# Optimization experiments

Measured on AMD Instinct MI355X. Metric: run time of the kernel, lower is better.

## Reference

```python
import jax, jax.numpy as jnp
import numpy as np

H = 1024
F = 4096  # base_ffn_dim = hidden * 4
WIDTHS = [256, 512]  # adapters; idx 2 -> width==hidden -> identity
EPS = 1e-5


def _xavier(key, fan_in, fan_out, gain):
    a = gain * np.sqrt(6.0 / (fan_in + fan_out))
    return jax.random.uniform(key, (fan_in, fan_out), jnp.float32, -a, a)


def _layernorm(x, g, b):
    mu = jnp.mean(x, axis=-1, keepdims=True)
    var = jnp.var(x, axis=-1, keepdims=True)
    return (x - mu) * jax.lax.rsqrt(var + EPS) * g + b


def setup_inputs() -> dict:
    key = jax.random.key(0)
    ks = jax.random.split(key, 12)
    g = 1.0 / np.sqrt(2.0)
    B, S = 4, 2048
    return {
        "x": jax.random.normal(ks[0], (B, S, H), jnp.float32),
        "width_multiplier": jax.random.uniform(ks[1], (B, S, 1), jnp.float32),
        "width_idx": jax.random.randint(ks[2], (B, S), 0, 3, jnp.int32),
        "ln_in_g": jnp.ones((H,), jnp.float32),
        "ln_in_b": jnp.zeros((H,), jnp.float32),
        "W1": _xavier(ks[3], H, F, g),
        "b1": jnp.zeros((F,), jnp.float32),
        "ln_h_g": jnp.ones((F,), jnp.float32),
        "ln_h_b": jnp.zeros((F,), jnp.float32),
        "W2": _xavier(ks[4], F, H, g),
        "b2": jnp.zeros((H,), jnp.float32),
        "a256_w1": _xavier(ks[5], H, 256, g),
        "a256_b1": jnp.zeros((256,), jnp.float32),
        "a256_w2": _xavier(ks[6], 256, H, g),
        "a256_b2": jnp.zeros((H,), jnp.float32),
        "a512_w1": _xavier(ks[7], H, 512, g),
        "a512_b1": jnp.zeros((512,), jnp.float32),
        "a512_w2": _xavier(ks[8], 512, H, g),
        "a512_b2": jnp.zeros((H,), jnp.float32),
    }


def reference(x, width_multiplier, width_idx,
              ln_in_g, ln_in_b, W1, b1, ln_h_g, ln_h_b, W2, b2,
              a256_w1, a256_b1, a256_w2, a256_b2,
              a512_w1, a512_b1, a512_w2, a512_b2):
    gelu = lambda t: jax.nn.gelu(t, approximate=False)  # torch nn.GELU exact
    x_norm = _layernorm(x, ln_in_g, ln_in_b)
    # base FFN path
    h = gelu(jnp.einsum("bsh,hf->bsf", x_norm, W1) + b1)
    h = _layernorm(h, ln_h_g, ln_h_b)
    base = jnp.einsum("bsf,fh->bsh", h, W2) + b2
    # width adapters (routed per token by width_idx)
    ad0 = jnp.einsum("bsw,wh->bsh", gelu(jnp.einsum("bsh,hw->bsw", x_norm, a256_w1) + a256_b1), a256_w2) + a256_b2
    ad1 = jnp.einsum("bsw,wh->bsh", gelu(jnp.einsum("bsh,hw->bsw", x_norm, a512_w1) + a512_b1), a512_w2) + a512_b2
    idx = width_idx[..., None]
    adaptive = jnp.where(idx == 0, ad0, jnp.where(idx == 1, ad1, x_norm))
    return base * width_multiplier + adaptive * (1.0 - width_multiplier)
```

## Files before the change

### kernel.cpp

```cpp
#include <hip/hip_runtime.h>
#include <cstdint>
#include <cstddef>

typedef unsigned short u16x8 __attribute__((ext_vector_type(8)));
typedef unsigned short u16x4 __attribute__((ext_vector_type(4)));
typedef __bf16 bf16x8 __attribute__((ext_vector_type(8)));
typedef float f32x4 __attribute__((ext_vector_type(4)));

__device__ __forceinline__ float b2f(unsigned short u) {
    union { unsigned int i; float f; } v;
    v.i = ((unsigned int)u) << 16;
    return v.f;
}

__device__ __forceinline__ unsigned short f2b(float f) {
    union { float f; unsigned int i; } v;
    v.f = f;
    unsigned int x = v.i;
    unsigned int lsb = (x >> 16) & 1u;
    x += 0x7FFFu + lsb;
    return (unsigned short)(x >> 16);
}

__device__ __forceinline__ float gelu_exact(float x) {
    return 0.5f * x * (1.0f + erff(x * 0.70710678118654752f));
}

__device__ __forceinline__ void ld_lds16(const unsigned short* g, unsigned short* l) {
    __builtin_amdgcn_global_load_lds(
        (const __attribute__((address_space(1))) void*)g,
        (__attribute__((address_space(3))) void*)l, 16, 0, 0);
}


__device__ __forceinline__ void transp_body(const float* __restrict__ in,
                                            unsigned short* __restrict__ out,
                                            int R, int C,
                                            const float* __restrict__ scale,
                                            int bx, int by) {
    __shared__ float tile[32][33];
    const int tx = threadIdx.x & 31;
    const int ty = threadIdx.x >> 5;
    int x = bx * 32 + tx;
    int y0 = by * 32;
    for (int k = 0; k < 32; k += 8)
        tile[ty + k][tx] = in[(size_t)(y0 + ty + k) * C + x];
    __syncthreads();
    int ox = y0 + tx;
    int oy = bx * 32;
    float sc = scale ? scale[ox] : 1.0f;
    for (int k = 0; k < 32; k += 8)
        out[(size_t)(oy + ty + k) * R + ox] = f2b(tile[tx][ty + k] * sc);
}

__device__ __forceinline__ void c01_partial_body(const float* __restrict__ W2,
                                                 const float* __restrict__ g,
                                                 const float* __restrict__ b,
                                                 float* __restrict__ pc0,
                                                 float* __restrict__ pc1,
                                                 int N, int kc, int nb) {
    int n = (nb << 8) + threadIdx.x;
    int k0 = kc << 8;
    float p0 = 0.f, p1 = 0.f;
    for (int k = k0; k < k0 + 256; ++k) {
        float w = W2[(size_t)k * N + n];
        p0 += b[k] * w;
        p1 += g[k] * w;
    }
    pc0[kc * 1024 + n] = p0;
    pc1[kc * 1024 + n] = p1;
}

__device__ __forceinline__ void ln1024_body(const float* __restrict__ in,
                                            unsigned short* __restrict__ out,
                                            const float* __restrict__ g,
                                            const float* __restrict__ b,
                                            int row) {
    const int t = threadIdx.x;
    f32x4 v = ((const f32x4*)(in + (size_t)row * 1024))[t];
    float s = v[0] + v[1] + v[2] + v[3];
    float s2 = v[0] * v[0] + v[1] * v[1] + v[2] * v[2] + v[3] * v[3];
#pragma unroll
    for (int o = 32; o > 0; o >>= 1) {
        s  += __shfl_down(s, o, 64);
        s2 += __shfl_down(s2, o, 64);
    }
    __shared__ float red[8];
    int lane = t & 63, w = t >> 6;
    if (lane == 0) { red[w] = s; red[4 + w] = s2; }
    __syncthreads();
    if (t == 0) {
        red[0] = red[0] + red[1] + red[2] + red[3];
        red[4] = red[4] + red[5] + red[6] + red[7];
    }
    __syncthreads();
    const float inv_n = 1.0f / 1024.0f;
    float mu = red[0] * inv_n;
    float var = red[4] * inv_n - mu * mu;
    float rs = rsqrtf(var + 1e-5f);
    f32x4 gv = ((const f32x4*)g)[t];
    f32x4 bv = ((const f32x4*)b)[t];
    u16x4 ov;
#pragma unroll
    for (int r = 0; r < 4; ++r) ov[r] = f2b((v[r] - mu) * rs * gv[r] + bv[r]);
    ((u16x4*)(out + (size_t)row * 1024))[t] = ov;
}

__device__ __forceinline__ void rowstats_body(const unsigned short* __restrict__ h,
                                              float* __restrict__ st, int row) {
    const int t = threadIdx.x;
    const u16x8* p = (const u16x8*)(h + (size_t)row * 4096);
    float s = 0.f, s2 = 0.f;
#pragma unroll
    for (int i = 0; i < 2; ++i) {
        u16x8 v = p[t + (i << 8)];
#pragma unroll
        for (int r = 0; r < 8; ++r) { float f = b2f(v[r]); s += f; s2 += f * f; }
    }
#pragma unroll
    for (int o = 32; o > 0; o >>= 1) {
        s  += __shfl_down(s, o, 64);
        s2 += __shfl_down(s2, o, 64);
    }
    __shared__ float red2[8];
    int lane = t & 63, w = t >> 6;
    if (lane == 0) { red2[w] = s; red2[4 + w] = s2; }
    __syncthreads();
    if (t == 0) {
        float ss = red2[0] + red2[1] + red2[2] + red2[3];
        float qq = red2[4] + red2[5] + red2[6] + red2[7];
        const float inv = 1.0f / 4096.0f;
        float mu = ss * inv;
        float var = qq * inv - mu * mu;
        float rs = rsqrtf(var + 1e-5f);
        st[2 * (size_t)row]     = rs;
        st[2 * (size_t)row + 1] = rs * mu;
    }
}

template <int EPI>
__device__ __forceinline__ void gemm_body(
    unsigned short (*As)[128 * 32], unsigned short (*Bs)[128 * 32],
    int fid, int nbx, int nby,
    const unsigned short* __restrict__ A, int lda,
    const unsigned short* __restrict__ BT, int ldb,
    const float* __restrict__ bias, unsigned short* __restrict__ Cb,
    float* __restrict__ Cf, int N, int K,
    const int* __restrict__ idx, int match,
    const float* __restrict__ wm,
    const unsigned short* __restrict__ adaptive,
    const unsigned short* __restrict__ xn,
    const float* __restrict__ c1v,
    const float* __restrict__ rstat) {
    const int t = threadIdx.x;

    int id = fid;
    const int nwg = nbx * nby;
    if ((nwg & 7) == 0) {
        const int cpx = nwg >> 3;
        id = (id & 7) * cpx + (id >> 3);
    }
    const int bx = id % nbx;
    const int by = id / nbx;
    const int m0 = by * 128;
    const int n0 = bx * 128;

    const int lane = t & 63;
    const int wid = t >> 6;

    const int srow = lane >> 2;
    const int sch  = (lane & 3) ^ (srow & 3);
    const int scol = sch << 3;

    const int wr = (wid >> 1) << 6;
    const int wc = (wid & 1) << 6;
    const int ml = lane & 15;
    const int q = lane >> 4;
    const int qsw = ((q ^ (ml & 3)) << 3);

    f32x4 acc[4][4];
#pragma unroll
    for (int i = 0; i < 4; ++i)
#pragma unroll
        for (int j = 0; j < 4; ++j)
#pragma unroll
            for (int r = 0; r < 4; ++r) acc[i][j][r] = 0.0f;

    const int nk = K >> 5;

#define STAGE(KT, BUF)                                                          \
    {                                                                           \
        _Pragma("unroll")                                                       \
        for (int hh = 0; hh < 2; ++hh) {                                        \
            int rbase = wid * 32 + hh * 16;                                     \
            int row = rbase + srow;                                             \
            ld_lds16(A  + (size_t)(m0 + row) * lda + (KT) * 32 + scol,          \
                     &As[BUF][rbase * 32]);                                     \
            ld_lds16(BT + (size_t)(n0 + row) * ldb + (KT) * 32 + scol,          \
                     &Bs[BUF][rbase * 32]);                                     \
        }                                                                       \
    }

    STAGE(0, 0);
    for (int kt = 0; kt < nk; ++kt) {
        const int cur = kt & 1;
        __syncthreads();
        if (kt + 1 < nk) STAGE(kt + 1, cur ^ 1);

        bf16x8 af[4], bf[4];
#pragma unroll
        for (int i = 0; i < 4; ++i)
            af[i] = *(const bf16x8*)(&As[cur][(wr + i * 16 + ml) * 32 + qsw]);
#pragma unroll
        for (int j = 0; j < 4; ++j)
            bf[j] = *(const bf16x8*)(&Bs[cur][(wc + j * 16 + ml) * 32 + qsw]);
#pragma unroll
        for (int i = 0; i < 4; ++i)
#pragma unroll
            for (int j = 0; j < 4; ++j)
                acc[i][j] = __builtin_amdgcn_mfma_f32_16x16x32_bf16(af[i], bf[j], acc[i][j], 0, 0, 0);
    }
#undef STAGE

#pragma unroll
    for (int i = 0; i < 4; ++i) {
        float rsv[4], rmv[4], wv[4];
        int idv[4];
        if (EPI == 1 || EPI == 2) {
#pragma unroll
            for (int r = 0; r < 4; ++r) {
                int row = m0 + wr + i * 16 + q * 4 + r;
                idv[r] = idx[row];
                if (EPI == 2) {
                    wv[r] = wm[row];
                    rsv[r] = rstat[2 * (size_t)row];
                    rmv[r] = rstat[2 * (size_t)row + 1];
                }
            }
        }
#pragma unroll
        for (int j = 0; j < 4; ++j) {
            int col = n0 + wc + j * 16 + ml;
            float bv = bias[col];
            float c1c = (EPI == 2) ? c1v[col] : 0.0f;
#pragma unroll
            for (int r = 0; r < 4; ++r) {
                int row = m0 + wr + i * 16 + q * 4 + r;
                size_t off = (size_t)row * N + col;
                if (EPI == 0) {
                    Cb[off] = f2b(gelu_exact(acc[i][j][r] + bv));
                } else if (EPI == 1) {
                    if (idv[r] == match) Cb[off] = f2b(acc[i][j][r] + bv);
                } else {
                    float bval = rsv[r] * acc[i][j][r] + bv - rmv[r] * c1c;
                    float a = b2f((idv[r] <= 1) ? adaptive[off] : xn[off]);
                    Cf[off] = bval * wv[r] + a * (1.0f - wv[r]);
                }
            }
        }
    }
}

__global__ __launch_bounds__(256) void mega_prep(
    const float* __restrict__ W1, const float* __restrict__ W2,
    const float* __restrict__ ln_h_g, const float* __restrict__ ln_h_b,
    const float* __restrict__ a256_w1, const float* __restrict__ a512_w1,
    const float* __restrict__ a256_w2, const float* __restrict__ a512_w2,
    const float* __restrict__ a256_b1, const float* __restrict__ a512_b1,
    const float* __restrict__ x, const float* __restrict__ ln_in_g,
    const float* __restrict__ ln_in_b,
    unsigned short* __restrict__ W1T, unsigned short* __restrict__ W2T,
    unsigned short* __restrict__ awup, unsigned short* __restrict__ aw2T0,
    unsigned short* __restrict__ aw2T1, float* __restrict__ ab1,
    float* __restrict__ pc0, float* __restrict__ pc1,
    unsigned short* __restrict__ xn) {
    const int H = 1024, F = 4096;
    int bid = blockIdx.x;
    if (bid < 4096) {
        transp_body(W1, W1T, H, F, nullptr, bid & 127, bid >> 7);
    } else if (bid < 8192) {
        int l = bid - 4096;
        transp_body(W2, W2T, F, H, ln_h_g, l & 31, l >> 5);
    } else if (bid < 8448) {
        int l = bid - 8192;
        transp_body(a256_w1, awup, H, 256, nullptr, l & 7, l >> 3);
    } else if (bid < 8960) {
        int l = bid - 8448;
        transp_body(a512_w1, awup + (size_t)256 * H, H, 512, nullptr, l & 15, l >> 4);
    } else if (bid < 9216) {
        int l = bid - 8960;
        transp_body(a256_w2, aw2T0, 256, H, nullptr, l & 31, l >> 5);
    } else if (bid < 9728) {
        int l = bid - 9216;
        transp_body(a512_w2, aw2T1, 512, H, nullptr, l & 31, l >> 5);
    } else if (bid < 9731) {
        int n = (bid - 9728) * 256 + threadIdx.x;
        if (n < 768) ab1[n] = (n < 256) ? a256_b1[n] : a512_b1[n - 256];
    } else if (bid < 9795) {
        int l = bid - 9731;
        c01_partial_body(W2, ln_h_g, ln_h_b, pc0, pc1, H, l >> 2, l & 3);
    } else {
        ln1024_body(x, xn, ln_in_g, ln_in_b, bid - 9795);
    }
}

template <int EPI>
__global__ __launch_bounds__(256) void gemm_bt(
    const unsigned short* __restrict__ A, int lda,
    const unsigned short* __restrict__ BT, int ldb,
    const float* __restrict__ bias, unsigned short* __restrict__ Cb,
    float* __restrict__ Cf, int N, int K,
    const int* __restrict__ idx, int match,
    const float* __restrict__ wm,
    const unsigned short* __restrict__ adaptive,
    const unsigned short* __restrict__ xn,
    const float* __restrict__ c1v,
    const float* __restrict__ rstat) {
    __shared__ __align__(16) unsigned short As[2][128 * 32];
    __shared__ __align__(16) unsigned short Bs[2][128 * 32];
    gemm_body<EPI>(As, Bs, blockIdx.y * gridDim.x + blockIdx.x,
                   gridDim.x, gridDim.y, A, lda, BT, ldb, bias, Cb, Cf, N, K,
                   idx, match, wm, adaptive, xn, c1v, rstat);
}

__global__ __launch_bounds__(256) void up_stats(
    const unsigned short* __restrict__ xn, const unsigned short* __restrict__ awup,
    const float* __restrict__ ab1, unsigned short* __restrict__ tt,
    const unsigned short* __restrict__ h, float* __restrict__ st) {
    __shared__ __align__(16) unsigned short As[2][128 * 32];
    __shared__ __align__(16) unsigned short Bs[2][128 * 32];
    int bid = blockIdx.x;
    if (bid < 384) {
        gemm_body<0>(As, Bs, bid, 6, 64, xn, 1024, awup, 1024, ab1, tt,
                     nullptr, 768, 1024, nullptr, 0, nullptr, nullptr, nullptr,
                     nullptr, nullptr);
    } else {
        rowstats_body(h, st, bid - 384);
    }
}

__global__ __launch_bounds__(256) void downs(
    const unsigned short* __restrict__ tt,
    const unsigned short* __restrict__ aw2T0, const unsigned short* __restrict__ aw2T1,
    const float* __restrict__ a256_b2, const float* __restrict__ a512_b2,
    unsigned short* __restrict__ adp, const int* __restrict__ widx,
    const float* __restrict__ pc0, const float* __restrict__ pc1,
    const float* __restrict__ b2, float* __restrict__ c0b2,
    float* __restrict__ c1) {
    __shared__ __align__(16) unsigned short As[2][128 * 32];
    __shared__ __align__(16) unsigned short Bs[2][128 * 32];
    int bid = blockIdx.x;
    if (bid < 512) {
        gemm_body<1>(As, Bs, bid, 8, 64, tt, 768, aw2T0, 256, a256_b2, adp,
                     nullptr, 1024, 256, widx, 0, nullptr, nullptr, nullptr,
                     nullptr, nullptr);
    } else if (bid < 1024) {
        gemm_body<1>(As, Bs, bid - 512, 8, 64, tt + 256, 768, aw2T1, 512,
                     a512_b2, adp, nullptr, 1024, 512, widx, 1, nullptr,
                     nullptr, nullptr, nullptr, nullptr);
    } else {
        int n = ((bid - 1024) << 8) + threadIdx.x;
        float s0 = b2[n], s1 = 0.f;
#pragma unroll
        for (int kc = 0; kc < 16; ++kc) {
            s0 += pc0[kc * 1024 + n];
            s1 += pc1[kc * 1024 + n];
        }
        c0b2[n] = s0;
        c1[n] = s1;
    }
}

extern "C" void kernel_launch(void* const* d_in, const int* in_sizes, int n_in,
                              void* d_out, int out_size, void* d_ws, size_t ws_size,
                              hipStream_t stream) {
    const float* x       = (const float*)d_in[0];
    const float* wm      = (const float*)d_in[1];
    const int*   widx    = (const int*)d_in[2];
    const float* ln_in_g = (const float*)d_in[3];
    const float* ln_in_b = (const float*)d_in[4];
    const float* W1      = (const float*)d_in[5];
    const float* b1      = (const float*)d_in[6];
    const float* ln_h_g  = (const float*)d_in[7];
    const float* ln_h_b  = (const float*)d_in[8];
    const float* W2      = (const float*)d_in[9];
    const float* b2      = (const float*)d_in[10];
    const float* a256_w1 = (const float*)d_in[11];
    const float* a256_b1 = (const float*)d_in[12];
    const float* a256_w2 = (const float*)d_in[13];
    const float* a256_b2 = (const float*)d_in[14];
    const float* a512_w1 = (const float*)d_in[15];
    const float* a512_b1 = (const float*)d_in[16];
    const float* a512_w2 = (const float*)d_in[17];
    const float* a512_b2 = (const float*)d_in[18];
    float* out = (float*)d_out;

    const int T = 8192, H = 1024, F = 4096;

    unsigned short* ws0   = (unsigned short*)d_ws;
    unsigned short* xn    = ws0;
    unsigned short* h     = xn    + (size_t)T * H;
    unsigned short* tt    = h     + (size_t)T * F;
    unsigned short* adp   = tt    + (size_t)T * 768;
    unsigned short* W1T   = adp   + (size_t)T * H;
    unsigned short* W2T   = W1T   + (size_t)H * F;
    unsigned short* awup  = W2T   + (size_t)F * H;
    unsigned short* aw2T0 = awup  + (size_t)768 * H;
    unsigned short* aw2T1 = aw2T0 + (size_t)H * 256;
    float*          ab1   = (float*)(aw2T1 + (size_t)H * 512);
    float*          stats = ab1 + 768;
    float*          c0b2  = stats + (size_t)T * 2;
    float*          c1    = c0b2 + H;
    float*          pc0   = c1 + H;
    float*          pc1   = pc0 + 16 * 1024;

    mega_prep<<<9795 + T, 256, 0, stream>>>(
        W1, W2, ln_h_g, ln_h_b, a256_w1, a512_w1, a256_w2, a512_w2,
        a256_b1, a512_b1, x, ln_in_g, ln_in_b,
        W1T, W2T, awup, aw2T0, aw2T1, ab1, pc0, pc1, xn);

    gemm_bt<0><<<dim3(F / 128, T / 128), 256, 0, stream>>>(
        xn, H, W1T, H, b1, h, nullptr, F, H, nullptr, 0, nullptr, nullptr,
        nullptr, nullptr, nullptr);

    up_stats<<<384 + T, 256, 0, stream>>>(xn, awup, ab1, tt, h, stats);

    downs<<<1028, 256, 0, stream>>>(tt, aw2T0, aw2T1, a256_b2, a512_b2, adp,
                                    widx, pc0, pc1, b2, c0b2, c1);

    gemm_bt<2><<<dim3(H / 128, T / 128), 256, 0, stream>>>(
        h, F, W2T, F, c0b2, nullptr, out, H, F, widx, 0, wm, adp, xn, c1, stats);
}
```

Baseline: 419.1 us.

## Fuse row stats into GEMM1 epilogue and merge adapter GEMMs into shared launches

The first FFN GEMM's epilogue now produces per-tile partial sums and sums of squares of the GELU output, so the separate pass that re-read h for LayerNorm statistics goes away; a small reduction in the middle kernel finalizes them. The adapter up-projection runs in the same launch as GEMM1, with routing-aware zeroing of the inactive half. The two adapter down-projections become one K=768 GEMM with a concatenated transposed weight and per-row bias selection. This cuts a kernel launch and a full read of the T×F h buffer, at the cost of extra epilogue shuffles and partial-sum storage, and the down GEMM now always does 768-deep work.

```diff
diff --git a/kernel.cpp b/kernel.cpp
--- a/kernel.cpp
+++ b/kernel.cpp
@@ -35,7 +35,7 @@
 
 __device__ __forceinline__ void transp_body(const float* __restrict__ in,
                                             unsigned short* __restrict__ out,
-                                            int R, int C,
+                                            int R, int C, int ldout,
                                             const float* __restrict__ scale,
                                             int bx, int by) {
     __shared__ float tile[32][33];
@@ -50,7 +50,7 @@
     int oy = bx * 32;
     float sc = scale ? scale[ox] : 1.0f;
     for (int k = 0; k < 32; k += 8)
-        out[(size_t)(oy + ty + k) * R + ox] = f2b(tile[tx][ty + k] * sc);
+        out[(size_t)(oy + ty + k) * ldout + ox] = f2b(tile[tx][ty + k] * sc);
 }
 
 __device__ __forceinline__ void c01_partial_body(const float* __restrict__ W2,
@@ -106,38 +106,6 @@
     ((u16x4*)(out + (size_t)row * 1024))[t] = ov;
 }
 
-__device__ __forceinline__ void rowstats_body(const unsigned short* __restrict__ h,
-                                              float* __restrict__ st, int row) {
-    const int t = threadIdx.x;
-    const u16x8* p = (const u16x8*)(h + (size_t)row * 4096);
-    float s = 0.f, s2 = 0.f;
-#pragma unroll
-    for (int i = 0; i < 2; ++i) {
-        u16x8 v = p[t + (i << 8)];
-#pragma unroll
-        for (int r = 0; r < 8; ++r) { float f = b2f(v[r]); s += f; s2 += f * f; }
-    }
-#pragma unroll
-    for (int o = 32; o > 0; o >>= 1) {
-        s  += __shfl_down(s, o, 64);
-        s2 += __shfl_down(s2, o, 64);
-    }
-    __shared__ float red2[8];
-    int lane = t & 63, w = t >> 6;
-    if (lane == 0) { red2[w] = s; red2[4 + w] = s2; }
-    __syncthreads();
-    if (t == 0) {
-        float ss = red2[0] + red2[1] + red2[2] + red2[3];
-        float qq = red2[4] + red2[5] + red2[6] + red2[7];
-        const float inv = 1.0f / 4096.0f;
-        float mu = ss * inv;
-        float var = qq * inv - mu * mu;
-        float rs = rsqrtf(var + 1e-5f);
-        st[2 * (size_t)row]     = rs;
-        st[2 * (size_t)row + 1] = rs * mu;
-    }
-}
-
 template <int EPI>
 __device__ __forceinline__ void gemm_body(
     unsigned short (*As)[128 * 32], unsigned short (*Bs)[128 * 32],
@@ -146,12 +114,13 @@
     const unsigned short* __restrict__ BT, int ldb,
     const float* __restrict__ bias, unsigned short* __restrict__ Cb,
     float* __restrict__ Cf, int N, int K,
-    const int* __restrict__ idx, int match,
+    const int* __restrict__ idx,
     const float* __restrict__ wm,
     const unsigned short* __restrict__ adaptive,
     const unsigned short* __restrict__ xn,
     const float* __restrict__ c1v,
-    const float* __restrict__ rstat) {
+    const float* __restrict__ rstat,
+    float* __restrict__ ps, float* __restrict__ pq) {
     const int t = threadIdx.x;
 
     int id = fid;
@@ -226,7 +195,12 @@
     for (int i = 0; i < 4; ++i) {
         float rsv[4], rmv[4], wv[4];
         int idv[4];
-        if (EPI == 1 || EPI == 2) {
+        float rsum[4], rqs[4];
+        if (EPI == 0) {
+#pragma unroll
+            for (int r = 0; r < 4; ++r) { rsum[r] = 0.f; rqs[r] = 0.f; }
+        }
+        if (EPI != 0) {
 #pragma unroll
             for (int r = 0; r < 4; ++r) {
                 int row = m0 + wr + i * 16 + q * 4 + r;
@@ -242,15 +216,23 @@
         for (int j = 0; j < 4; ++j) {
             int col = n0 + wc + j * 16 + ml;
             float bv = bias[col];
+            float bv1 = (EPI == 4) ? bias[1024 + col] : 0.0f;
             float c1c = (EPI == 2) ? c1v[col] : 0.0f;
 #pragma unroll
             for (int r = 0; r < 4; ++r) {
                 int row = m0 + wr + i * 16 + q * 4 + r;
                 size_t off = (size_t)row * N + col;
                 if (EPI == 0) {
-                    Cb[off] = f2b(gelu_exact(acc[i][j][r] + bv));
-                } else if (EPI == 1) {
-                    if (idv[r] == match) Cb[off] = f2b(acc[i][j][r] + bv);
+                    float g = gelu_exact(acc[i][j][r] + bv);
+                    Cb[off] = f2b(g);
+                    rsum[r] += g;
+                    rqs[r] += g * g;
+                } else if (EPI == 3) {
+                    bool act = (col < 256) ? (idv[r] == 0) : (idv[r] == 1);
+                    Cb[off] = f2b(act ? gelu_exact(acc[i][j][r] + bv) : 0.0f);
+                } else if (EPI == 4) {
+                    float bsel = (idv[r] == 1) ? bv1 : bv;
+                    Cb[off] = f2b(acc[i][j][r] + bsel);
                 } else {
                     float bval = rsv[r] * acc[i][j][r] + bv - rmv[r] * c1c;
                     float a = b2f((idv[r] <= 1) ? adaptive[off] : xn[off]);
@@ -258,6 +240,22 @@
                 }
             }
         }
+        if (EPI == 0) {
+#pragma unroll
+            for (int r = 0; r < 4; ++r) {
+                float s = rsum[r], s2 = rqs[r];
+                s  += __shfl_xor(s, 1);  s2 += __shfl_xor(s2, 1);
+                s  += __shfl_xor(s, 2);  s2 += __shfl_xor(s2, 2);
+                s  += __shfl_xor(s, 4);  s2 += __shfl_xor(s2, 4);
+                s  += __shfl_xor(s, 8);  s2 += __shfl_xor(s2, 8);
+                if (ml == 0) {
+                    int row = m0 + wr + i * 16 + q * 4 + r;
+                    size_t pidx = (size_t)row * 64 + ((n0 + wc) >> 6);
+                    ps[pidx] = s;
+                    pq[pidx] = s2;
+                }
+            }
+        }
     }
 }
 
@@ -267,83 +265,73 @@
     const float* __restrict__ a256_w1, const float* __restrict__ a512_w1,
     const float* __restrict__ a256_w2, const float* __restrict__ a512_w2,
     const float* __restrict__ a256_b1, const float* __restrict__ a512_b1,
+    const float* __restrict__ a256_b2, const float* __restrict__ a512_b2,
     const float* __restrict__ x, const float* __restrict__ ln_in_g,
     const float* __restrict__ ln_in_b,
     unsigned short* __restrict__ W1T, unsigned short* __restrict__ W2T,
-    unsigned short* __restrict__ awup, unsigned short* __restrict__ aw2T0,
-    unsigned short* __restrict__ aw2T1, float* __restrict__ ab1,
+    unsigned short* __restrict__ awup, unsigned short* __restrict__ awdT,
+    float* __restrict__ ab1, float* __restrict__ b2sel,
     float* __restrict__ pc0, float* __restrict__ pc1,
     unsigned short* __restrict__ xn) {
     const int H = 1024, F = 4096;
     int bid = blockIdx.x;
     if (bid < 4096) {
-        transp_body(W1, W1T, H, F, nullptr, bid & 127, bid >> 7);
+        transp_body(W1, W1T, H, F, H, nullptr, bid & 127, bid >> 7);
     } else if (bid < 8192) {
         int l = bid - 4096;
-        transp_body(W2, W2T, F, H, ln_h_g, l & 31, l >> 5);
+        transp_body(W2, W2T, F, H, F, ln_h_g, l & 31, l >> 5);
     } else if (bid < 8448) {
         int l = bid - 8192;
-        transp_body(a256_w1, awup, H, 256, nullptr, l & 7, l >> 3);
+        transp_body(a256_w1, awup, H, 256, H, nullptr, l & 7, l >> 3);
     } else if (bid < 8960) {
         int l = bid - 8448;
-        transp_body(a512_w1, awup + (size_t)256 * H, H, 512, nullptr, l & 15, l >> 4);
+        transp_body(a512_w1, awup + (size_t)256 * H, H, 512, H, nullptr, l & 15, l >> 4);
     } else if (bid < 9216) {
         int l = bid - 8960;
-        transp_body(a256_w2, aw2T0, 256, H, nullptr, l & 31, l >> 5);
+        transp_body(a256_w2, awdT, 256, H, 768, nullptr, l & 31, l >> 5);
     } else if (bid < 9728) {
         int l = bid - 9216;
-        transp_body(a512_w2, aw2T1, 512, H, nullptr, l & 31, l >> 5);
+        transp_body(a512_w2, awdT + 256, 512, H, 768, nullptr, l & 31, l >> 5);
     } else if (bid < 9731) {
         int n = (bid - 9728) * 256 + threadIdx.x;
         if (n < 768) ab1[n] = (n < 256) ? a256_b1[n] : a512_b1[n - 256];
-    } else if (bid < 9795) {
-        int l = bid - 9731;
+    } else if (bid < 9739) {
+        int n = (bid - 9731) * 256 + threadIdx.x;
+        b2sel[n] = (n < 1024) ? a256_b2[n] : a512_b2[n - 1024];
+    } else if (bid < 9803) {
+        int l = bid - 9739;
         c01_partial_body(W2, ln_h_g, ln_h_b, pc0, pc1, H, l >> 2, l & 3);
     } else {
-        ln1024_body(x, xn, ln_in_g, ln_in_b, bid - 9795);
-    }
-}
-
-template <int EPI>
-__global__ __launch_bounds__(256) void gemm_bt(
-    const unsigned short* __restrict__ A, int lda,
-    const unsigned short* __restrict__ BT, int ldb,
-    const float* __restrict__ bias, unsigned short* __restrict__ Cb,
-    float* __restrict__ Cf, int N, int K,
-    const int* __restrict__ idx, int match,
-    const float* __restrict__ wm,
-    const unsigned short* __restrict__ adaptive,
-    const unsigned short* __restrict__ xn,
-    const float* __restrict__ c1v,
-    const float* __restrict__ rstat) {
-    __shared__ __align__(16) unsigned short As[2][128 * 32];
-    __shared__ __align__(16) unsigned short Bs[2][128 * 32];
-    gemm_body<EPI>(As, Bs, blockIdx.y * gridDim.x + blockIdx.x,
-                   gridDim.x, gridDim.y, A, lda, BT, ldb, bias, Cb, Cf, N, K,
-                   idx, match, wm, adaptive, xn, c1v, rstat);
-}
-
-__global__ __launch_bounds__(256) void up_stats(
-    const unsigned short* __restrict__ xn, const unsigned short* __restrict__ awup,
-    const float* __restrict__ ab1, unsigned short* __restrict__ tt,
-    const unsigned short* __restrict__ h, float* __restrict__ st) {
+        ln1024_body(x, xn, ln_in_g, ln_in_b, bid - 9803);
+    }
+}
+
+__global__ __launch_bounds__(256) void big1(
+    const unsigned short* __restrict__ xn, const unsigned short* __restrict__ W1T,
+    const float* __restrict__ b1, unsigned short* __restrict__ h,
+    float* __restrict__ ps, float* __restrict__ pq,
+    const unsigned short* __restrict__ awup, const float* __restrict__ ab1,
+    unsigned short* __restrict__ tt, const int* __restrict__ widx) {
     __shared__ __align__(16) unsigned short As[2][128 * 32];
     __shared__ __align__(16) unsigned short Bs[2][128 * 32];
     int bid = blockIdx.x;
-    if (bid < 384) {
-        gemm_body<0>(As, Bs, bid, 6, 64, xn, 1024, awup, 1024, ab1, tt,
-                     nullptr, 768, 1024, nullptr, 0, nullptr, nullptr, nullptr,
-                     nullptr, nullptr);
+    if (bid < 2048) {
+        gemm_body<0>(As, Bs, bid, 32, 64, xn, 1024, W1T, 1024, b1, h,
+                     nullptr, 4096, 1024, nullptr, nullptr, nullptr, nullptr,
+                     nullptr, nullptr, ps, pq);
     } else {
-        rowstats_body(h, st, bid - 384);
-    }
-}
-
-__global__ __launch_bounds__(256) void downs(
-    const unsigned short* __restrict__ tt,
-    const unsigned short* __restrict__ aw2T0, const unsigned short* __restrict__ aw2T1,
-    const float* __restrict__ a256_b2, const float* __restrict__ a512_b2,
-    unsigned short* __restrict__ adp, const int* __restrict__ widx,
+        gemm_body<3>(As, Bs, bid - 2048, 6, 64, xn, 1024, awup, 1024, ab1, tt,
+                     nullptr, 768, 1024, widx, nullptr, nullptr, nullptr,
+                     nullptr, nullptr, nullptr, nullptr);
+    }
+}
+
+__global__ __launch_bounds__(256) void mid_k(
+    const unsigned short* __restrict__ tt, const unsigned short* __restrict__ awdT,
+    const float* __restrict__ b2sel, unsigned short* __restrict__ adp,
+    const int* __restrict__ widx,
+    const float* __restrict__ ps, const float* __restrict__ pq,
+    float* __restrict__ stats,
     const float* __restrict__ pc0, const float* __restrict__ pc1,
     const float* __restrict__ b2, float* __restrict__ c0b2,
     float* __restrict__ c1) {
@@ -351,15 +339,24 @@
     __shared__ __align__(16) unsigned short Bs[2][128 * 32];
     int bid = blockIdx.x;
     if (bid < 512) {
-        gemm_body<1>(As, Bs, bid, 8, 64, tt, 768, aw2T0, 256, a256_b2, adp,
-                     nullptr, 1024, 256, widx, 0, nullptr, nullptr, nullptr,
-                     nullptr, nullptr);
-    } else if (bid < 1024) {
-        gemm_body<1>(As, Bs, bid - 512, 8, 64, tt + 256, 768, aw2T1, 512,
-                     a512_b2, adp, nullptr, 1024, 512, widx, 1, nullptr,
+        gemm_body<4>(As, Bs, bid, 8, 64, tt, 768, awdT, 768, b2sel, adp,
+                     nullptr, 1024, 768, widx, nullptr, nullptr, nullptr,
                      nullptr, nullptr, nullptr, nullptr);
+    } else if (bid < 544) {
+        int row = (bid - 512) * 256 + threadIdx.x;
+        float s0 = 0.f, s1 = 0.f;
+        const float* pr = ps + (size_t)row * 64;
+        const float* qr = pq + (size_t)row * 64;
+#pragma unroll
+        for (int c = 0; c < 64; ++c) { s0 += pr[c]; s1 += qr[c]; }
+        const float inv = 1.0f / 4096.0f;
+        float mu = s0 * inv;
+        float var = s1 * inv - mu * mu;
+        float rs = rsqrtf(var + 1e-5f);
+        stats[2 * (size_t)row]     = rs;
+        stats[2 * (size_t)row + 1] = rs * mu;
     } else {
-        int n = ((bid - 1024) << 8) + threadIdx.x;
+        int n = ((bid - 544) << 8) + threadIdx.x;
         float s0 = b2[n], s1 = 0.f;
 #pragma unroll
         for (int kc = 0; kc < 16; ++kc) {
@@ -369,6 +366,21 @@
         c0b2[n] = s0;
         c1[n] = s1;
     }
+}
+
+__global__ __launch_bounds__(256) void gemm_fin(
+    const unsigned short* __restrict__ A, int lda,
+    const unsigned short* __restrict__ BT, int ldb,
+    const float* __restrict__ bias, float* __restrict__ Cf, int N, int K,
+    const int* __restrict__ idx, const float* __restrict__ wm,
+    const unsigned short* __restrict__ adaptive,
+    const unsigned short* __restrict__ xn,
+    const float* __restrict__ c1v, const float* __restrict__ rstat) {
+    __shared__ __align__(16) unsigned short As[2][128 * 32];
+    __shared__ __align__(16) unsigned short Bs[2][128 * 32];
+    gemm_body<2>(As, Bs, blockIdx.y * gridDim.x + blockIdx.x,
+                 gridDim.x, gridDim.y, A, lda, BT, ldb, bias, nullptr, Cf, N, K,
+                 idx, wm, adaptive, xn, c1v, rstat, nullptr, nullptr);
 }
 
 extern "C" void kernel_launch(void* const* d_in, const int* in_sizes, int n_in,
@@ -405,29 +417,28 @@
     unsigned short* W1T   = adp   + (size_t)T * H;
     unsigned short* W2T   = W1T   + (size_t)H * F;
     unsigned short* awup  = W2T   + (size_t)F * H;
-    unsigned short* aw2T0 = awup  + (size_t)768 * H;
-    unsigned short* aw2T1 = aw2T0 + (size_t)H * 256;
-    float*          ab1   = (float*)(aw2T1 + (size_t)H * 512);
-    float*          stats = ab1 + 768;
+    unsigned short* awdT  = awup  + (size_t)768 * H;
+    float*          ab1   = (float*)(awdT + (size_t)H * 768);
+    float*          b2sel = ab1 + 768;
+    float*          stats = b2sel + 2048;
     float*          c0b2  = stats + (size_t)T * 2;
     float*          c1    = c0b2 + H;
     float*          pc0   = c1 + H;
     float*          pc1   = pc0 + 16 * 1024;
-
-    mega_prep<<<9795 + T, 256, 0, stream>>>(
+    float*          ps    = pc1 + 16 * 1024;
+    float*          pq    = ps + (size_t)T * 64;
+
+    mega_prep<<<9803 + T, 256, 0, stream>>>(
         W1, W2, ln_h_g, ln_h_b, a256_w1, a512_w1, a256_w2, a512_w2,
-        a256_b1, a512_b1, x, ln_in_g, ln_in_b,
-        W1T, W2T, awup, aw2T0, aw2T1, ab1, pc0, pc1, xn);
-
-    gemm_bt<0><<<dim3(F / 128, T / 128), 256, 0, stream>>>(
-        xn, H, W1T, H, b1, h, nullptr, F, H, nullptr, 0, nullptr, nullptr,
-        nullptr, nullptr, nullptr);
-
-    up_stats<<<384 + T, 256, 0, stream>>>(xn, awup, ab1, tt, h, stats);
-
-    downs<<<1028, 256, 0, stream>>>(tt, aw2T0, aw2T1, a256_b2, a512_b2, adp,
-                                    widx, pc0, pc1, b2, c0b2, c1);
-
-    gemm_bt<2><<<dim3(H / 128, T / 128), 256, 0, stream>>>(
-        h, F, W2T, F, c0b2, nullptr, out, H, F, widx, 0, wm, adp, xn, c1, stats);
-}
+        a256_b1, a512_b1, a256_b2, a512_b2, x, ln_in_g, ln_in_b,
+        W1T, W2T, awup, awdT, ab1, b2sel, pc0, pc1, xn);
+
+    big1<<<2048 + 384, 256, 0, stream>>>(
+        xn, W1T, b1, h, ps, pq, awup, ab1, tt, widx);
+
+    mid_k<<<512 + 32 + 4, 256, 0, stream>>>(
+        tt, awdT, b2sel, adp, widx, ps, pq, stats, pc0, pc1, b2, c0b2, c1);
+
+    gemm_fin<<<dim3(H / 128, T / 128), 256, 0, stream>>>(
+        h, F, W2T, F, c0b2, out, H, F, widx, wm, adp, xn, c1, stats);
+}
```

After: 444.2 us. +6.0%, slower.
